# Kernel tuning notes

Hardware: AMD Instinct MI355X
Metric: run time of the kernel (lower is better)

Reference implementation:

```python
import jax, jax.numpy as jnp
import numpy as np

B, T, D, H = 2, 2048, 1024, 16
HS = D // H  # head_size = 64
EPS = 1e-5


def layer_norm(x, g, b):
    mu = jnp.mean(x, axis=-1, keepdims=True)
    var = jnp.var(x, axis=-1, keepdims=True)
    return (x - mu) * jax.lax.rsqrt(var + EPS) * g + b


def setup_inputs() -> dict:
    key = jax.random.key(0)
    ks = jax.random.split(key, 12)
    s_attn = 1.0 / np.sqrt(D)
    s_ff1 = 1.0 / np.sqrt(D)
    s_ff2 = 1.0 / np.sqrt(4 * D)
    return {
        "x": jax.random.normal(ks[0], (B, T, D), jnp.float32),
        "Wq": jax.random.normal(ks[1], (H, D, HS), jnp.float32) * s_attn,
        "Wk": jax.random.normal(ks[2], (H, D, HS), jnp.float32) * s_attn,
        "Wv": jax.random.normal(ks[3], (H, D, HS), jnp.float32) * s_attn,
        "Wo": jax.random.normal(ks[4], (H * HS, D), jnp.float32) * (1.0 / np.sqrt(H * HS)),
        "bo": jnp.zeros((D,), jnp.float32),
        "W1": jax.random.normal(ks[5], (D, 4 * D), jnp.float32) * s_ff1,
        "b1": jnp.zeros((4 * D,), jnp.float32),
        "W2": jax.random.normal(ks[6], (4 * D, D), jnp.float32) * s_ff2,
        "b2": jnp.zeros((D,), jnp.float32),
        "ln1_g": jnp.ones((D,), jnp.float32),
        "ln1_b": jnp.zeros((D,), jnp.float32),
        "ln2_g": jnp.ones((D,), jnp.float32),
        "ln2_b": jnp.zeros((D,), jnp.float32),
    }


def reference(x, Wq, Wk, Wv, Wo, bo, W1, b1, W2, b2, ln1_g, ln1_b, ln2_g, ln2_b):
    # --- self-attention on ln1(x) ---
    h = layer_norm(x, ln1_g, ln1_b)
    Q = jnp.einsum('bsd,hdk->bhsk', h, Wq)
    K = jnp.einsum('bsd,hdk->bhsk', h, Wk)
    V = jnp.einsum('bsd,hdk->bhsk', h, Wv)
    scores = jnp.einsum('bhqk,bhsk->bhqs', Q, K) * (HS ** -0.5)
    attn = jax.nn.softmax(scores, axis=-1)  # [B,H,T,T] non-causal, as in source
    out = jnp.einsum('bhqs,bhsk->bhqk', attn, V)
    out = out.transpose(0, 2, 1, 3).reshape(B, T, H * HS)  # concat heads
    sa = out @ Wo + bo
    x = x + sa
    # --- feed-forward on ln2(x) ---
    h2 = layer_norm(x, ln2_g, ln2_b)
    ff = jax.nn.relu(h2 @ W1 + b1) @ W2 + b2
    return x + ff
```

## Files before the change

kernel.cpp:

```cpp
#include <hip/hip_runtime.h>
#include <cstdint>
#include <cmath>

typedef __bf16 bf16;
typedef __bf16 bf16x8 __attribute__((ext_vector_type(8)));
typedef __bf16 bf16x4 __attribute__((ext_vector_type(4)));
typedef __bf16 bf16x2 __attribute__((ext_vector_type(2)));
typedef float  f32x4  __attribute__((ext_vector_type(4)));

#define B_   2
#define T_   2048
#define D_   1024
#define H_   16
#define HS_  64
#define NTOK (B_ * T_)

typedef __attribute__((address_space(1))) uint8_t* gp1_t;
typedef __attribute__((address_space(3))) uint8_t* lp3_t;
__device__ __forceinline__ void gl_lds16(const void* g, void* l) {
    __builtin_amdgcn_global_load_lds((gp1_t)(uintptr_t)g,
                                     (lp3_t)(uint32_t)(uintptr_t)l,
                                     16, 0, 0);
}

__device__ __forceinline__ f32x4 mfma16(bf16x8 a, bf16x8 b, f32x4 c) {
    return __builtin_amdgcn_mfma_f32_16x16x32_bf16(a, b, c, 0, 0, 0);
}

__device__ __forceinline__ uint32_t pk2(float lo, float hi) {
    uint32_t r;
    asm("v_cvt_pk_bf16_f32 %0, %1, %2" : "=v"(r) : "v"(lo), "v"(hi));
    return r;
}
__device__ __forceinline__ void pl32(uint32_t& a, uint32_t& b) {
    asm("v_permlane32_swap_b32 %0, %1" : "+v"(a), "+v"(b));
}
__device__ __forceinline__ void pl16(uint32_t& a, uint32_t& b) {
    asm("v_permlane16_swap_b32 %0, %1" : "+v"(a), "+v"(b));
}

__global__ __launch_bounds__(256) void prep_fused(
    const float* __restrict__ Wq, const float* __restrict__ Wk,
    const float* __restrict__ Wv, const float* __restrict__ Wo,
    const float* __restrict__ W1, const float* __restrict__ W2,
    const float* __restrict__ x,  const float* __restrict__ g,
    const float* __restrict__ be,
    bf16* __restrict__ WqkvT, bf16* __restrict__ WoT,
    bf16* __restrict__ W1T,  bf16* __restrict__ W2T,
    bf16* __restrict__ hbuf) {
    const int bid = blockIdx.x;
    const int tid = threadIdx.x;

    if (bid >= 12288) {
        const int row = bid - 12288;
        const float4 v = ((const float4*)(x + (size_t)row * 1024))[tid];
        float s  = v.x + v.y + v.z + v.w;
        float s2 = v.x * v.x + v.y * v.y + v.z * v.z + v.w * v.w;
        for (int m = 1; m < 64; m <<= 1) {
            s  += __shfl_xor(s, m);
            s2 += __shfl_xor(s2, m);
        }
        __shared__ float rs[4], rq[4];
        const int lane = tid & 63, wv = tid >> 6;
        if (lane == 0) { rs[wv] = s; rq[wv] = s2; }
        __syncthreads();
        s  = rs[0] + rs[1] + rs[2] + rs[3];
        s2 = rq[0] + rq[1] + rq[2] + rq[3];
        const float mu   = s * (1.f / 1024.f);
        const float var  = s2 * (1.f / 1024.f) - mu * mu;
        const float rstd = rsqrtf(var + 1e-5f);
        const float4 gg = ((const float4*)g)[tid];
        const float4 bb = ((const float4*)be)[tid];
        bf16x4 o;
        o[0] = (bf16)((v.x - mu) * rstd * gg.x + bb.x);
        o[1] = (bf16)((v.y - mu) * rstd * gg.y + bb.y);
        o[2] = (bf16)((v.z - mu) * rstd * gg.z + bb.z);
        o[3] = (bf16)((v.w - mu) * rstd * gg.w + bb.w);
        *(bf16x4*)(hbuf + (size_t)row * 1024 + tid * 4) = o;
        return;
    }

    const float* in; bf16* out;
    int C, R, bx, by;
    if (bid < 3072) {
        const int z = bid >> 6, rem = bid & 63;
        bx = rem & 1; by = rem >> 1;
        C = HS_; R = D_;
        in  = (z < 16 ? Wq : z < 32 ? Wk : Wv) + (size_t)(z & 15) * D_ * HS_;
        out = WqkvT + (size_t)z * HS_ * D_;
    } else if (bid < 4096) {
        const int rem = bid - 3072;
        bx = rem & 31; by = rem >> 5;
        C = 1024; R = 1024; in = Wo; out = WoT;
    } else if (bid < 8192) {
        const int rem = bid - 4096;
        bx = rem & 127; by = rem >> 7;
        C = 4096; R = 1024; in = W1; out = W1T;
    } else {
        const int rem = bid - 8192;
        bx = rem & 31; by = rem >> 5;
        C = 1024; R = 4096; in = W2; out = W2T;
    }
    const int tx = tid & 31, ty = tid >> 5;
    const int c0 = bx * 32, r0 = by * 32;
    __shared__ float t[32][33];
    for (int i = 0; i < 4; i++) {
        int r = ty + i * 8;
        t[r][tx] = in[(size_t)(r0 + r) * C + c0 + tx];
    }
    __syncthreads();
    for (int i = 0; i < 4; i++) {
        int rr = ty + i * 8;
        out[(size_t)(c0 + rr) * R + r0 + tx] = (bf16)t[tx][rr];
    }
}

__global__ __launch_bounds__(256) void ln_kernel(const float* __restrict__ x,
                                                 const float* __restrict__ g,
                                                 const float* __restrict__ b,
                                                 bf16* __restrict__ out) {
    const int row = blockIdx.x;
    const int tid = threadIdx.x;
    const float4 v = ((const float4*)(x + (size_t)row * 1024))[tid];
    float s  = v.x + v.y + v.z + v.w;
    float s2 = v.x * v.x + v.y * v.y + v.z * v.z + v.w * v.w;
    for (int m = 1; m < 64; m <<= 1) {
        s  += __shfl_xor(s, m);
        s2 += __shfl_xor(s2, m);
    }
    __shared__ float rs[4], rq[4];
    const int lane = tid & 63, wv = tid >> 6;
    if (lane == 0) { rs[wv] = s; rq[wv] = s2; }
    __syncthreads();
    s  = rs[0] + rs[1] + rs[2] + rs[3];
    s2 = rq[0] + rq[1] + rq[2] + rq[3];
    const float mu   = s * (1.f / 1024.f);
    const float var  = s2 * (1.f / 1024.f) - mu * mu;
    const float rstd = rsqrtf(var + 1e-5f);
    const float4 gg = ((const float4*)g)[tid];
    const float4 bb = ((const float4*)b)[tid];
    bf16x4 o;
    o[0] = (bf16)((v.x - mu) * rstd * gg.x + bb.x);
    o[1] = (bf16)((v.y - mu) * rstd * gg.y + bb.y);
    o[2] = (bf16)((v.z - mu) * rstd * gg.z + bb.z);
    o[3] = (bf16)((v.w - mu) * rstd * gg.w + bb.w);
    *(bf16x4*)(out + (size_t)row * 1024 + tid * 4) = o;
}

template <int BIAS, int RELU, int RES, int OUTBF16, int VTP = 0>
__global__ __launch_bounds__(256, 2) void gemm128v2(
    const bf16* __restrict__ A, const bf16* __restrict__ Bt,
    const float* __restrict__ bias, const float* __restrict__ resid,
    void* __restrict__ Cout, bf16* __restrict__ Vt, int M, int N, int K) {
    __shared__ __align__(16) bf16 Asub[4][128 * 32];
    __shared__ __align__(16) bf16 Bsub[4][128 * 32];
    const int tid  = threadIdx.x;
    const int lane = tid & 63, w = tid >> 6;
    const int quad = lane >> 4, l15 = lane & 15;
    const int m0 = blockIdx.y * 128, n0 = blockIdx.x * 128;
    const int wm = (w & 1) * 64, wn = (w >> 1) * 64;
    const int S  = K / 32;

    const int slog = (((lane & 3) ^ ((lane >> 3) & 3)) * 8);
    const int crow = lane >> 2;
    const bf16* gA0 = A  + (size_t)(m0 + 32 * w + crow)      * K + slog;
    const bf16* gA1 = A  + (size_t)(m0 + 32 * w + 16 + crow) * K + slog;
    const bf16* gB0 = Bt + (size_t)(n0 + 32 * w + crow)      * K + slog;
    const bf16* gB1 = Bt + (size_t)(n0 + 32 * w + 16 + crow) * K + slog;

    for (int t = 0; t < 3; t++) {
        gl_lds16(gA0, &Asub[t][(32 * w) * 32]);
        gl_lds16(gA1, &Asub[t][(32 * w + 16) * 32]);
        gl_lds16(gB0, &Bsub[t][(32 * w) * 32]);
        gl_lds16(gB1, &Bsub[t][(32 * w + 16) * 32]);
        gA0 += 32; gA1 += 32; gB0 += 32; gB1 += 32;
    }

    f32x4 acc[4][4];
#pragma unroll
    for (int i = 0; i < 4; i++)
#pragma unroll
        for (int j = 0; j < 4; j++) acc[i][j] = f32x4{0.f, 0.f, 0.f, 0.f};

    const int swz = (quad ^ ((l15 >> 1) & 3)) * 8;
    const int aof = (wm + l15) * 32 + swz;
    const int bof = (wn + l15) * 32 + swz;

    asm volatile("s_waitcnt vmcnt(8)" ::: "memory");
    __builtin_amdgcn_sched_barrier(0);
    __builtin_amdgcn_s_barrier();

    for (int s = 0; s < S; s++) {
        const bf16* Ab = &Asub[s & 3][0];
        const bf16* Bb = &Bsub[s & 3][0];
        const int pb = (s + 3) & 3;
        bf16x8 af[4], bfr[4];
#pragma unroll
        for (int mi = 0; mi < 4; mi++) af[mi] = *(const bf16x8*)&Ab[aof + mi * 512];
#pragma unroll
        for (int ni = 0; ni < 4; ni++) bfr[ni] = *(const bf16x8*)&Bb[bof + ni * 512];
        if (s + 3 < S) {
            gl_lds16(gA0, &Asub[pb][(32 * w) * 32]);
            gl_lds16(gA1, &Asub[pb][(32 * w + 16) * 32]);
            gl_lds16(gB0, &Bsub[pb][(32 * w) * 32]);
            gl_lds16(gB1, &Bsub[pb][(32 * w + 16) * 32]);
            gA0 += 32; gA1 += 32; gB0 += 32; gB1 += 32;
        }
        asm volatile("s_waitcnt lgkmcnt(0)" ::: "memory");
        __builtin_amdgcn_sched_barrier(0);
        __builtin_amdgcn_s_setprio(1);
#pragma unroll
        for (int mi = 0; mi < 4; mi++)
#pragma unroll
            for (int ni = 0; ni < 4; ni++)
                acc[mi][ni] = mfma16(af[mi], bfr[ni], acc[mi][ni]);
        __builtin_amdgcn_s_setprio(0);
        __builtin_amdgcn_sched_barrier(0);
        if (s <= S - 4)      asm volatile("s_waitcnt vmcnt(8)" ::: "memory");
        else if (s == S - 3) asm volatile("s_waitcnt vmcnt(4)" ::: "memory");
        else if (s == S - 2) asm volatile("s_waitcnt vmcnt(0)" ::: "memory");
        __builtin_amdgcn_s_barrier();
    }

    for (int mi = 0; mi < 4; mi++) {
        for (int ni = 0; ni < 4; ni++) {
            const int colb = n0 + wn + ni * 16 + l15;
            if (VTP && colb >= 2048) {
                const int h = (colb - 2048) >> 6, hs = (colb - 2048) & 63;
                const int row0 = m0 + wm + mi * 16 + quad * 4;
                const int b = row0 >> 11;
                bf16x4 p4;
                p4[0] = (bf16)acc[mi][ni][0];
                p4[1] = (bf16)acc[mi][ni][1];
                p4[2] = (bf16)acc[mi][ni][2];
                p4[3] = (bf16)acc[mi][ni][3];
                *(bf16x4*)&Vt[((size_t)(b * 16 + h) * 64 + hs) * T_ + (row0 & 2047)] = p4;
                continue;
            }
            const float bv = BIAS ? bias[colb] : 0.f;
            for (int r = 0; r < 4; r++) {
                const int row = m0 + wm + mi * 16 + quad * 4 + r;
                float v = acc[mi][ni][r] + bv;
                if (RELU) v = fmaxf(v, 0.f);
                if (RES)  v += resid[(size_t)row * N + colb];
                if (OUTBF16) ((bf16*)Cout)[(size_t)row * N + colb] = (bf16)v;
                else         ((float*)Cout)[(size_t)row * N + colb] = v;
            }
        }
    }
}

template <int BIAS, int RELU, int RES, int OUTBF16>
__global__ __launch_bounds__(256, 2) void gemm64n(
    const bf16* __restrict__ A, const bf16* __restrict__ Bt,
    const float* __restrict__ bias, const float* __restrict__ resid,
    void* __restrict__ Cout, int M, int N, int K) {
    __shared__ __align__(16) bf16 Asub[4][128 * 32];
    __shared__ __align__(16) bf16 Bsub[4][64 * 32];
    const int tid  = threadIdx.x;
    const int lane = tid & 63, w = tid >> 6;
    const int quad = lane >> 4, l15 = lane & 15;
    const int m0 = blockIdx.y * 128, n0 = blockIdx.x * 64;
    const int wm = (w & 1) * 64, wn = (w >> 1) * 32;
    const int S  = K / 32;

    const int slog = (((lane & 3) ^ ((lane >> 3) & 3)) * 8);
    const int crow = lane >> 2;
    const bf16* gA0 = A  + (size_t)(m0 + 32 * w + crow)      * K + slog;
    const bf16* gA1 = A  + (size_t)(m0 + 32 * w + 16 + crow) * K + slog;
    const bf16* gB0 = Bt + (size_t)(n0 + 16 * w + crow)      * K + slog;

    for (int t = 0; t < 3; t++) {
        gl_lds16(gA0, &Asub[t][(32 * w) * 32]);
        gl_lds16(gA1, &Asub[t][(32 * w + 16) * 32]);
        gl_lds16(gB0, &Bsub[t][(16 * w) * 32]);
        gA0 += 32; gA1 += 32; gB0 += 32;
    }

    f32x4 acc[4][2];
#pragma unroll
    for (int i = 0; i < 4; i++)
#pragma unroll
        for (int j = 0; j < 2; j++) acc[i][j] = f32x4{0.f, 0.f, 0.f, 0.f};

    const int swz = (quad ^ ((l15 >> 1) & 3)) * 8;
    const int aof = (wm + l15) * 32 + swz;
    const int bof = (wn + l15) * 32 + swz;

    asm volatile("s_waitcnt vmcnt(6)" ::: "memory");
    __builtin_amdgcn_sched_barrier(0);
    __builtin_amdgcn_s_barrier();

    for (int s = 0; s < S; s++) {
        const bf16* Ab = &Asub[s & 3][0];
        const bf16* Bb = &Bsub[s & 3][0];
        const int pb = (s + 3) & 3;
        bf16x8 af[4], bfr[2];
#pragma unroll
        for (int mi = 0; mi < 4; mi++) af[mi] = *(const bf16x8*)&Ab[aof + mi * 512];
#pragma unroll
        for (int ni = 0; ni < 2; ni++) bfr[ni] = *(const bf16x8*)&Bb[bof + ni * 512];
        if (s + 3 < S) {
            gl_lds16(gA0, &Asub[pb][(32 * w) * 32]);
            gl_lds16(gA1, &Asub[pb][(32 * w + 16) * 32]);
            gl_lds16(gB0, &Bsub[pb][(16 * w) * 32]);
            gA0 += 32; gA1 += 32; gB0 += 32;
        }
        asm volatile("s_waitcnt lgkmcnt(0)" ::: "memory");
        __builtin_amdgcn_sched_barrier(0);
        __builtin_amdgcn_s_setprio(1);
#pragma unroll
        for (int mi = 0; mi < 4; mi++)
#pragma unroll
            for (int ni = 0; ni < 2; ni++)
                acc[mi][ni] = mfma16(af[mi], bfr[ni], acc[mi][ni]);
        __builtin_amdgcn_s_setprio(0);
        __builtin_amdgcn_sched_barrier(0);
        if (s <= S - 4)      asm volatile("s_waitcnt vmcnt(6)" ::: "memory");
        else if (s == S - 3) asm volatile("s_waitcnt vmcnt(3)" ::: "memory");
        else if (s == S - 2) asm volatile("s_waitcnt vmcnt(0)" ::: "memory");
        __builtin_amdgcn_s_barrier();
    }

    for (int mi = 0; mi < 4; mi++) {
        for (int ni = 0; ni < 2; ni++) {
            const int colb = n0 + wn + ni * 16 + l15;
            const float bv = BIAS ? bias[colb] : 0.f;
            for (int r = 0; r < 4; r++) {
                const int row = m0 + wm + mi * 16 + quad * 4 + r;
                float v = acc[mi][ni][r] + bv;
                if (RELU) v = fmaxf(v, 0.f);
                if (RES)  v += resid[(size_t)row * N + colb];
                if (OUTBF16) ((bf16*)Cout)[(size_t)row * N + colb] = (bf16)v;
                else         ((float*)Cout)[(size_t)row * N + colb] = v;
            }
        }
    }
}

template <int BIAS, int RELU>
__global__ __launch_bounds__(512, 2) void gemm256(
    const bf16* __restrict__ A, const bf16* __restrict__ Bt,
    const float* __restrict__ bias, void* __restrict__ Cout,
    int M, int N, int K) {
    __shared__ __align__(16) bf16 Asub[4][256 * 32];
    __shared__ __align__(16) bf16 Bsub[4][256 * 32];
    const int tid  = threadIdx.x;
    const int lane = tid & 63, w = tid >> 6;
    const int wr = w >> 2, wc = w & 3;
    const int quad = lane >> 4, l15 = lane & 15;
    const int m0 = blockIdx.y * 256, n0 = blockIdx.x * 256;
    const int S   = K / 32;

    const int slog = (((lane & 3) ^ ((lane >> 3) & 3)) * 8);
    const int crow = lane >> 2;
    const bf16* gA0 = A  + (size_t)(m0 + 32 * w + crow)      * K + slog;
    const bf16* gA1 = A  + (size_t)(m0 + 32 * w + 16 + crow) * K + slog;
    const bf16* gB0 = Bt + (size_t)(n0 + 32 * w + crow)      * K + slog;
    const bf16* gB1 = Bt + (size_t)(n0 + 32 * w + 16 + crow) * K + slog;

    for (int t = 0; t < 3; t++) {
        gl_lds16(gA0, &Asub[t][(32 * w) * 32]);
        gl_lds16(gA1, &Asub[t][(32 * w + 16) * 32]);
        gl_lds16(gB0, &Bsub[t][(32 * w) * 32]);
        gl_lds16(gB1, &Bsub[t][(32 * w + 16) * 32]);
        gA0 += 32; gA1 += 32; gB0 += 32; gB1 += 32;
    }

    f32x4 acc[8][4];
#pragma unroll
    for (int i = 0; i < 8; i++)
#pragma unroll
        for (int j = 0; j < 4; j++) acc[i][j] = f32x4{0.f, 0.f, 0.f, 0.f};

    const int swz = (quad ^ ((l15 >> 1) & 3)) * 8;
    const int aof = (wr * 128 + l15) * 32 + swz;
    const int bof = (wc * 64 + l15) * 32 + swz;

    asm volatile("s_waitcnt vmcnt(8)" ::: "memory");
    __builtin_amdgcn_sched_barrier(0);
    __builtin_amdgcn_s_barrier();

    for (int s = 0; s < S; s++) {
        const bf16* Ab = &Asub[s & 3][0];
        const bf16* Bb = &Bsub[s & 3][0];
        const int pb = (s + 3) & 3;
        bf16x8 af[4], bfr[4];
#pragma unroll
        for (int f = 0; f < 4; f++) af[f] = *(const bf16x8*)&Ab[aof + f * 512];
#pragma unroll
        for (int n = 0; n < 4; n++) bfr[n] = *(const bf16x8*)&Bb[bof + n * 512];
        if (s + 3 < S) {
            gl_lds16(gA0, &Asub[pb][(32 * w) * 32]);
            gl_lds16(gA1, &Asub[pb][(32 * w + 16) * 32]);
            gA0 += 32; gA1 += 32;
        }
        asm volatile("s_waitcnt lgkmcnt(0)" ::: "memory");
        __builtin_amdgcn_sched_barrier(0);
        __builtin_amdgcn_s_setprio(1);
#pragma unroll
        for (int f = 0; f < 4; f++)
#pragma unroll
            for (int n = 0; n < 4; n++)
                acc[f][n] = mfma16(af[f], bfr[n], acc[f][n]);
        __builtin_amdgcn_s_setprio(0);
#pragma unroll
        for (int f = 0; f < 4; f++) af[f] = *(const bf16x8*)&Ab[aof + 2048 + f * 512];
        if (s + 3 < S) {
            gl_lds16(gB0, &Bsub[pb][(32 * w) * 32]);
            gl_lds16(gB1, &Bsub[pb][(32 * w + 16) * 32]);
            gB0 += 32; gB1 += 32;
        }
        asm volatile("s_waitcnt lgkmcnt(0)" ::: "memory");
        __builtin_amdgcn_sched_barrier(0);
        __builtin_amdgcn_s_setprio(1);
#pragma unroll
        for (int f = 0; f < 4; f++)
#pragma unroll
            for (int n = 0; n < 4; n++)
                acc[4 + f][n] = mfma16(af[f], bfr[n], acc[4 + f][n]);
        __builtin_amdgcn_s_setprio(0);
        __builtin_amdgcn_sched_barrier(0);
        if (s <= S - 4)      asm volatile("s_waitcnt vmcnt(8)" ::: "memory");
        else if (s == S - 3) asm volatile("s_waitcnt vmcnt(4)" ::: "memory");
        else if (s == S - 2) asm volatile("s_waitcnt vmcnt(0)" ::: "memory");
        __builtin_amdgcn_s_barrier();
    }

#pragma unroll
    for (int mi = 0; mi < 8; mi++) {
#pragma unroll
        for (int ni = 0; ni < 4; ni++) {
            const int colb = n0 + wc * 64 + ni * 16 + l15;
            const int row0 = m0 + wr * 128 + (mi >> 2) * 64 + (mi & 3) * 16 + quad * 4;
            const float bv = BIAS ? bias[colb] : 0.f;
            for (int r = 0; r < 4; r++) {
                float v = acc[mi][ni][r] + bv;
                if (RELU) v = fmaxf(v, 0.f);
                ((bf16*)Cout)[(size_t)(row0 + r) * N + colb] = (bf16)v;
            }
        }
    }
}

#define LSTR 68
#define NJ   (T_ / 64)
__global__ __launch_bounds__(256, 2) void flash_attn(const bf16* __restrict__ QKV,
                                                     const bf16* __restrict__ Vt,
                                                     bf16* __restrict__ attn_out) {
    const int bh = blockIdx.y, b = bh >> 4, h = bh & 15;
    const int q0 = blockIdx.x * 128;
    const int tid = threadIdx.x, lane = tid & 63, w = tid >> 6;
    const int quad = lane >> 4, l15 = lane & 15;
    __shared__ __align__(16) bf16 Ks[2][64 * LSTR];
    __shared__ __align__(16) bf16 Vs[2][64 * LSTR];
    const bf16* Qb = QKV + (size_t)b * T_ * 3072 + h * 64;
    const bf16* Kb = QKV + (size_t)b * T_ * 3072 + 1024 + h * 64;
    const bf16* Vb = Vt  + (size_t)bh * HS_ * T_;

    const float sc = 0.125f * 1.44269504088896f;
    const int sr = tid >> 2, scc = (tid & 3) * 16;

    bf16x8 QA[2][2];
    for (int qnt = 0; qnt < 2; qnt++) {
        const size_t row = (size_t)(q0 + w * 32 + qnt * 16 + l15) * 3072;
        for (int kk = 0; kk < 2; kk++) {
            bf16x8 q = *(const bf16x8*)&Qb[row + kk * 32 + quad * 8];
            for (int i = 0; i < 8; i++) q[i] = (bf16)((float)q[i] * sc);
            QA[qnt][kk] = q;
        }
    }

    bf16x8 ones8;
    for (int i = 0; i < 8; i++) ones8[i] = (bf16)1.0f;

    f32x4 O[2][4], lacc[2];
    for (int mi = 0; mi < 2; mi++) {
        lacc[mi] = f32x4{0.f, 0.f, 0.f, 0.f};
        for (int n = 0; n < 4; n++) O[mi][n] = f32x4{0.f, 0.f, 0.f, 0.f};
    }

    *(bf16x8*)&Ks[0][sr * LSTR + scc]     = *(const bf16x8*)&Kb[(size_t)sr * 3072 + scc];
    *(bf16x8*)&Ks[0][sr * LSTR + scc + 8] = *(const bf16x8*)&Kb[(size_t)sr * 3072 + scc + 8];
    *(bf16x8*)&Vs[0][sr * LSTR + scc]     = *(const bf16x8*)&Vb[(size_t)sr * T_ + scc];
    *(bf16x8*)&Vs[0][sr * LSTR + scc + 8] = *(const bf16x8*)&Vb[(size_t)sr * T_ + scc + 8];
    __syncthreads();

    bf16x8 k0, k1, v0, v1;
    for (int j = 0; j < NJ; j++) {
        const int buf = j & 1;
        if (j + 1 < NJ) {
            const int s1 = (j + 1) * 64;
            k0 = *(const bf16x8*)&Kb[(size_t)(s1 + sr) * 3072 + scc];
            k1 = *(const bf16x8*)&Kb[(size_t)(s1 + sr) * 3072 + scc + 8];
            v0 = *(const bf16x8*)&Vb[(size_t)sr * T_ + s1 + scc];
            v1 = *(const bf16x8*)&Vb[(size_t)sr * T_ + s1 + scc + 8];
        }
        bf16x8 KB[4][2];
#pragma unroll
        for (int smt = 0; smt < 4; smt++)
#pragma unroll
            for (int kk = 0; kk < 2; kk++)
                KB[smt][kk] = *(const bf16x8*)&Ks[buf][(smt * 16 + l15) * LSTR + kk * 32 + quad * 8];

        bf16x8 PA[2][2];
#pragma unroll
        for (int qnt = 0; qnt < 2; qnt++) {
            f32x4 ST[4];
#pragma unroll
            for (int smt = 0; smt < 4; smt++) ST[smt] = f32x4{0.f, 0.f, 0.f, 0.f};
            __builtin_amdgcn_s_setprio(1);
#pragma unroll
            for (int kk = 0; kk < 2; kk++)
#pragma unroll
                for (int smt = 0; smt < 4; smt++)
                    ST[smt] = mfma16(KB[smt][kk], QA[qnt][kk], ST[smt]);
            __builtin_amdgcn_s_setprio(0);
            uint32_t w00 = pk2(__builtin_amdgcn_exp2f(ST[0][0]), __builtin_amdgcn_exp2f(ST[0][1]));
            uint32_t w01 = pk2(__builtin_amdgcn_exp2f(ST[0][2]), __builtin_amdgcn_exp2f(ST[0][3]));
            uint32_t w10 = pk2(__builtin_amdgcn_exp2f(ST[1][0]), __builtin_amdgcn_exp2f(ST[1][1]));
            uint32_t w11 = pk2(__builtin_amdgcn_exp2f(ST[1][2]), __builtin_amdgcn_exp2f(ST[1][3]));
            uint32_t w20 = pk2(__builtin_amdgcn_exp2f(ST[2][0]), __builtin_amdgcn_exp2f(ST[2][1]));
            uint32_t w21 = pk2(__builtin_amdgcn_exp2f(ST[2][2]), __builtin_amdgcn_exp2f(ST[2][3]));
            uint32_t w30 = pk2(__builtin_amdgcn_exp2f(ST[3][0]), __builtin_amdgcn_exp2f(ST[3][1]));
            uint32_t w31 = pk2(__builtin_amdgcn_exp2f(ST[3][2]), __builtin_amdgcn_exp2f(ST[3][3]));
            pl32(w00, w10); pl16(w00, w10);
            pl32(w01, w11); pl16(w01, w11);
            pl32(w20, w30); pl16(w20, w30);
            pl32(w21, w31); pl16(w21, w31);
            union { uint32_t u[4]; bf16x8 v; } pa0, pa1;
            pa0.u[0] = w00; pa0.u[1] = w01; pa0.u[2] = w10; pa0.u[3] = w11;
            pa1.u[0] = w20; pa1.u[1] = w21; pa1.u[2] = w30; pa1.u[3] = w31;
            PA[qnt][0] = pa0.v;
            PA[qnt][1] = pa1.v;
        }
        bf16x8 VB[4][2];
#pragma unroll
        for (int n = 0; n < 4; n++)
#pragma unroll
            for (int kk = 0; kk < 2; kk++)
                VB[n][kk] = *(const bf16x8*)&Vs[buf][(n * 16 + l15) * LSTR + kk * 32 + quad * 8];
        __builtin_amdgcn_s_setprio(1);
#pragma unroll
        for (int mi = 0; mi < 2; mi++) {
            const bf16x8 PA0 = PA[mi][0];
            const bf16x8 PA1 = PA[mi][1];
#pragma unroll
            for (int n = 0; n < 4; n++) {
                O[mi][n] = mfma16(PA0, VB[n][0], O[mi][n]);
                O[mi][n] = mfma16(PA1, VB[n][1], O[mi][n]);
            }
            lacc[mi] = mfma16(PA0, ones8, lacc[mi]);
            lacc[mi] = mfma16(PA1, ones8, lacc[mi]);
        }
        __builtin_amdgcn_s_setprio(0);
        if (j + 1 < NJ) {
            *(bf16x8*)&Ks[buf ^ 1][sr * LSTR + scc]     = k0;
            *(bf16x8*)&Ks[buf ^ 1][sr * LSTR + scc + 8] = k1;
            *(bf16x8*)&Vs[buf ^ 1][sr * LSTR + scc]     = v0;
            *(bf16x8*)&Vs[buf ^ 1][sr * LSTR + scc + 8] = v1;
        }
        __syncthreads();
    }

    for (int mi = 0; mi < 2; mi++) {
        for (int r = 0; r < 4; r++) {
            const float inv = 1.f / lacc[mi][r];
            const size_t tok = (size_t)b * T_ + q0 + w * 32 + mi * 16 + quad * 4 + r;
            for (int n = 0; n < 4; n++)
                attn_out[tok * 1024 + h * 64 + n * 16 + l15] = (bf16)(O[mi][n][r] * inv);
        }
    }
}

extern "C" void kernel_launch(void* const* d_in, const int* in_sizes, int n_in,
                              void* d_out, int out_size, void* d_ws, size_t ws_size,
                              hipStream_t stream) {
    const float* x   = (const float*)d_in[0];
    const float* Wq  = (const float*)d_in[1];
    const float* Wk  = (const float*)d_in[2];
    const float* Wv  = (const float*)d_in[3];
    const float* Wo  = (const float*)d_in[4];
    const float* bo  = (const float*)d_in[5];
    const float* W1  = (const float*)d_in[6];
    const float* b1  = (const float*)d_in[7];
    const float* W2  = (const float*)d_in[8];
    const float* b2  = (const float*)d_in[9];
    const float* g1  = (const float*)d_in[10];
    const float* be1 = (const float*)d_in[11];
    const float* g2  = (const float*)d_in[12];
    const float* be2 = (const float*)d_in[13];

    char* ws = (char*)d_ws;
    const size_t MB = 1ull << 20;
    bf16*  WqkvT = (bf16*)(ws);
    bf16*  WoT   = (bf16*)(ws + 6  * MB);
    bf16*  W1T   = (bf16*)(ws + 8  * MB);
    bf16*  W2T   = (bf16*)(ws + 16 * MB);
    bf16*  hbuf  = (bf16*)(ws + 24 * MB);
    bf16*  QKV   = (bf16*)(ws + 32 * MB);
    bf16*  Vt    = (bf16*)(ws + 56 * MB);
    bf16*  attn  = (bf16*)(ws + 64 * MB);
    float* x2    = (float*)(ws + 72 * MB);
    bf16*  ff1   = (bf16*)(ws + 32 * MB);
    float* out   = (float*)d_out;

    prep_fused<<<16384, 256, 0, stream>>>(Wq, Wk, Wv, Wo, W1, W2, x, g1, be1,
                                          WqkvT, WoT, W1T, W2T, hbuf);
    gemm128v2<0, 0, 0, 1, 1><<<dim3(24, 32), 256, 0, stream>>>(
        hbuf, WqkvT, nullptr, nullptr, QKV, Vt, NTOK, 3072, 1024);
    flash_attn<<<dim3(T_ / 128, B_ * H_), 256, 0, stream>>>(QKV, Vt, attn);
    gemm64n<1, 0, 1, 0><<<dim3(16, 32), 256, 0, stream>>>(
        attn, WoT, bo, x, x2, NTOK, 1024, 1024);
    ln_kernel<<<NTOK, 256, 0, stream>>>(x2, g2, be2, hbuf);
    gemm256<1, 1><<<dim3(16, 16), 512, 0, stream>>>(
        hbuf, W1T, b1, ff1, NTOK, 4096, 1024);
    gemm64n<1, 0, 1, 0><<<dim3(16, 32), 256, 0, stream>>>(
        ff1, W2T, b2, x2, out, NTOK, 1024, 4096);
}
```

Before: 321.2 us.

## Use split-K 128x128 GEMM for FFN down-projection and 128-tile GEMM for Wo

Replaces the 128x64-tile GEMM for the W2 projection with a 128x128-tile split-K kernel (K split in two) that writes fp32 partials, then a new combine kernel adds both partials, the residual and the bias. The Wo projection switches from the 128x64-tile kernel to the existing 128x128 gemm128v2 with a fused epilogue. Larger tiles raise operand reuse, and split-K keeps the grid at 512 blocks for the long-K GEMM. The cost is 32 MB of extra fp32 partial traffic and one more launch, and the Wo GEMM now runs only 256 blocks.

```diff
diff --git a/kernel.cpp b/kernel.cpp
--- a/kernel.cpp
+++ b/kernel.cpp
@@ -145,6 +145,24 @@
     o[2] = (bf16)((v.z - mu) * rstd * gg.z + bb.z);
     o[3] = (bf16)((v.w - mu) * rstd * gg.w + bb.w);
     *(bf16x4*)(out + (size_t)row * 1024 + tid * 4) = o;
+}
+
+__global__ __launch_bounds__(256) void combine2(const float* __restrict__ p0,
+                                                const float* __restrict__ p1,
+                                                const float* __restrict__ resid,
+                                                const float* __restrict__ bias,
+                                                float* __restrict__ out) {
+    const int i4 = blockIdx.x * 256 + threadIdx.x;
+    const float4 a = ((const float4*)p0)[i4];
+    const float4 b = ((const float4*)p1)[i4];
+    const float4 r = ((const float4*)resid)[i4];
+    const float4 bb = ((const float4*)bias)[i4 & 255];
+    float4 o;
+    o.x = a.x + b.x + r.x + bb.x;
+    o.y = a.y + b.y + r.y + bb.y;
+    o.z = a.z + b.z + r.z + bb.z;
+    o.w = a.w + b.w + r.w + bb.w;
+    ((float4*)out)[i4] = o;
 }
 
 template <int BIAS, int RELU, int RES, int OUTBF16, int VTP = 0>
@@ -250,44 +268,47 @@
     }
 }
 
-template <int BIAS, int RELU, int RES, int OUTBF16>
-__global__ __launch_bounds__(256, 2) void gemm64n(
+__global__ __launch_bounds__(256, 2) void gemm128sk(
     const bf16* __restrict__ A, const bf16* __restrict__ Bt,
-    const float* __restrict__ bias, const float* __restrict__ resid,
-    void* __restrict__ Cout, int M, int N, int K) {
+    float* __restrict__ Cpart, int M, int N, int K) {
     __shared__ __align__(16) bf16 Asub[4][128 * 32];
-    __shared__ __align__(16) bf16 Bsub[4][64 * 32];
+    __shared__ __align__(16) bf16 Bsub[4][128 * 32];
     const int tid  = threadIdx.x;
     const int lane = tid & 63, w = tid >> 6;
     const int quad = lane >> 4, l15 = lane & 15;
-    const int m0 = blockIdx.y * 128, n0 = blockIdx.x * 64;
-    const int wm = (w & 1) * 64, wn = (w >> 1) * 32;
-    const int S  = K / 32;
+    const int m0 = blockIdx.y * 128, n0 = blockIdx.x * 128;
+    const int wm = (w & 1) * 64, wn = (w >> 1) * 64;
+    const int kpb = K / (int)gridDim.z;
+    const int k0  = (int)blockIdx.z * kpb;
+    const int S   = kpb / 32;
+    float* Cz = Cpart + (size_t)blockIdx.z * M * N;
 
     const int slog = (((lane & 3) ^ ((lane >> 3) & 3)) * 8);
     const int crow = lane >> 2;
-    const bf16* gA0 = A  + (size_t)(m0 + 32 * w + crow)      * K + slog;
-    const bf16* gA1 = A  + (size_t)(m0 + 32 * w + 16 + crow) * K + slog;
-    const bf16* gB0 = Bt + (size_t)(n0 + 16 * w + crow)      * K + slog;
+    const bf16* gA0 = A  + (size_t)(m0 + 32 * w + crow)      * K + k0 + slog;
+    const bf16* gA1 = A  + (size_t)(m0 + 32 * w + 16 + crow) * K + k0 + slog;
+    const bf16* gB0 = Bt + (size_t)(n0 + 32 * w + crow)      * K + k0 + slog;
+    const bf16* gB1 = Bt + (size_t)(n0 + 32 * w + 16 + crow) * K + k0 + slog;
 
     for (int t = 0; t < 3; t++) {
         gl_lds16(gA0, &Asub[t][(32 * w) * 32]);
         gl_lds16(gA1, &Asub[t][(32 * w + 16) * 32]);
-        gl_lds16(gB0, &Bsub[t][(16 * w) * 32]);
-        gA0 += 32; gA1 += 32; gB0 += 32;
-    }
-
-    f32x4 acc[4][2];
+        gl_lds16(gB0, &Bsub[t][(32 * w) * 32]);
+        gl_lds16(gB1, &Bsub[t][(32 * w + 16) * 32]);
+        gA0 += 32; gA1 += 32; gB0 += 32; gB1 += 32;
+    }
+
+    f32x4 acc[4][4];
 #pragma unroll
     for (int i = 0; i < 4; i++)
 #pragma unroll
-        for (int j = 0; j < 2; j++) acc[i][j] = f32x4{0.f, 0.f, 0.f, 0.f};
+        for (int j = 0; j < 4; j++) acc[i][j] = f32x4{0.f, 0.f, 0.f, 0.f};
 
     const int swz = (quad ^ ((l15 >> 1) & 3)) * 8;
     const int aof = (wm + l15) * 32 + swz;
     const int bof = (wn + l15) * 32 + swz;
 
-    asm volatile("s_waitcnt vmcnt(6)" ::: "memory");
+    asm volatile("s_waitcnt vmcnt(8)" ::: "memory");
     __builtin_amdgcn_sched_barrier(0);
     __builtin_amdgcn_s_barrier();
 
@@ -295,16 +316,17 @@
         const bf16* Ab = &Asub[s & 3][0];
         const bf16* Bb = &Bsub[s & 3][0];
         const int pb = (s + 3) & 3;
-        bf16x8 af[4], bfr[2];
+        bf16x8 af[4], bfr[4];
 #pragma unroll
         for (int mi = 0; mi < 4; mi++) af[mi] = *(const bf16x8*)&Ab[aof + mi * 512];
 #pragma unroll
-        for (int ni = 0; ni < 2; ni++) bfr[ni] = *(const bf16x8*)&Bb[bof + ni * 512];
+        for (int ni = 0; ni < 4; ni++) bfr[ni] = *(const bf16x8*)&Bb[bof + ni * 512];
         if (s + 3 < S) {
             gl_lds16(gA0, &Asub[pb][(32 * w) * 32]);
             gl_lds16(gA1, &Asub[pb][(32 * w + 16) * 32]);
-            gl_lds16(gB0, &Bsub[pb][(16 * w) * 32]);
-            gA0 += 32; gA1 += 32; gB0 += 32;
+            gl_lds16(gB0, &Bsub[pb][(32 * w) * 32]);
+            gl_lds16(gB1, &Bsub[pb][(32 * w + 16) * 32]);
+            gA0 += 32; gA1 += 32; gB0 += 32; gB1 += 32;
         }
         asm volatile("s_waitcnt lgkmcnt(0)" ::: "memory");
         __builtin_amdgcn_sched_barrier(0);
@@ -312,27 +334,22 @@
 #pragma unroll
         for (int mi = 0; mi < 4; mi++)
 #pragma unroll
-            for (int ni = 0; ni < 2; ni++)
+            for (int ni = 0; ni < 4; ni++)
                 acc[mi][ni] = mfma16(af[mi], bfr[ni], acc[mi][ni]);
         __builtin_amdgcn_s_setprio(0);
         __builtin_amdgcn_sched_barrier(0);
-        if (s <= S - 4)      asm volatile("s_waitcnt vmcnt(6)" ::: "memory");
-        else if (s == S - 3) asm volatile("s_waitcnt vmcnt(3)" ::: "memory");
+        if (s <= S - 4)      asm volatile("s_waitcnt vmcnt(8)" ::: "memory");
+        else if (s == S - 3) asm volatile("s_waitcnt vmcnt(4)" ::: "memory");
         else if (s == S - 2) asm volatile("s_waitcnt vmcnt(0)" ::: "memory");
         __builtin_amdgcn_s_barrier();
     }
 
     for (int mi = 0; mi < 4; mi++) {
-        for (int ni = 0; ni < 2; ni++) {
+        for (int ni = 0; ni < 4; ni++) {
             const int colb = n0 + wn + ni * 16 + l15;
-            const float bv = BIAS ? bias[colb] : 0.f;
             for (int r = 0; r < 4; r++) {
                 const int row = m0 + wm + mi * 16 + quad * 4 + r;
-                float v = acc[mi][ni][r] + bv;
-                if (RELU) v = fmaxf(v, 0.f);
-                if (RES)  v += resid[(size_t)row * N + colb];
-                if (OUTBF16) ((bf16*)Cout)[(size_t)row * N + colb] = (bf16)v;
-                else         ((float*)Cout)[(size_t)row * N + colb] = v;
+                Cz[(size_t)row * N + colb] = acc[mi][ni][r];
             }
         }
     }
@@ -603,6 +620,7 @@
     bf16*  attn  = (bf16*)(ws + 64 * MB);
     float* x2    = (float*)(ws + 72 * MB);
     bf16*  ff1   = (bf16*)(ws + 32 * MB);
+    float* part  = (float*)(ws + 88 * MB);
     float* out   = (float*)d_out;
 
     prep_fused<<<16384, 256, 0, stream>>>(Wq, Wk, Wv, Wo, W1, W2, x, g1, be1,
@@ -610,11 +628,13 @@
     gemm128v2<0, 0, 0, 1, 1><<<dim3(24, 32), 256, 0, stream>>>(
         hbuf, WqkvT, nullptr, nullptr, QKV, Vt, NTOK, 3072, 1024);
     flash_attn<<<dim3(T_ / 128, B_ * H_), 256, 0, stream>>>(QKV, Vt, attn);
-    gemm64n<1, 0, 1, 0><<<dim3(16, 32), 256, 0, stream>>>(
-        attn, WoT, bo, x, x2, NTOK, 1024, 1024);
+    gemm128v2<1, 0, 1, 0><<<dim3(8, 32), 256, 0, stream>>>(
+        attn, WoT, bo, x, x2, nullptr, NTOK, 1024, 1024);
     ln_kernel<<<NTOK, 256, 0, stream>>>(x2, g2, be2, hbuf);
     gemm256<1, 1><<<dim3(16, 16), 512, 0, stream>>>(
         hbuf, W1T, b1, ff1, NTOK, 4096, 1024);
-    gemm64n<1, 0, 1, 0><<<dim3(16, 32), 256, 0, stream>>>(
-        ff1, W2T, b2, x2, out, NTOK, 1024, 4096);
-}
+    gemm128sk<<<dim3(8, 32, 2), 256, 0, stream>>>(
+        ff1, W2T, part, NTOK, 1024, 4096);
+    combine2<<<NTOK, 256, 0, stream>>>(part, part + (size_t)NTOK * 1024,
+                                       x2, b2, out);
+}
```

New measurement: 320.8 us. No clear change (-0.1%).
